# Kernel optimization log

Measured on AMD Instinct MI355X. Metric: run time of the kernel, lower is better.

The kernel has to match this reference:

```python
import jax, jax.numpy as jnp
import numpy as np
import math

B, C, H, W = 8, 64, 256, 256
E, NH = 256, 8
HD = E // NH  # 32


def get_coords(h, w):
    xx, yy = jnp.meshgrid(jnp.arange(h, dtype=jnp.float32), jnp.arange(w, dtype=jnp.float32), indexing='ij')
    return jnp.stack((xx.reshape(-1), yy.reshape(-1)), axis=-1)  # [N, 2]


def setup_inputs() -> dict:
    key = jax.random.key(0)
    ks = jax.random.split(key, 12)
    def xavier(k, shape):
        fan_out, fan_in = shape
        a = math.sqrt(6.0 / (fan_in + fan_out))
        return jax.random.uniform(k, shape, jnp.float32, -a, a)
    x = jax.random.normal(ks[0], (B, C, H, W), jnp.float32)
    z = jax.random.normal(ks[1], (B, C), jnp.float32)
    pos = jax.random.uniform(ks[2], (B, NH, 2), jnp.float32) * (H - 1)
    Wq = xavier(ks[3], (E, C)); bq = jnp.zeros((E,), jnp.float32)
    Wk = xavier(ks[4], (E, C)); bk = jnp.zeros((E,), jnp.float32)
    Wv = xavier(ks[5], (E, C)); bv = jnp.zeros((E,), jnp.float32)
    Wp = xavier(ks[6], (HD, 2)); bp = jax.random.uniform(ks[7], (HD,), jnp.float32, -1.0, 1.0) / math.sqrt(2.0)
    return {"x": x, "z": z, "pos": pos, "Wq": Wq, "bq": bq, "Wk": Wk, "bk": bk,
            "Wv": Wv, "bv": bv, "Wp": Wp, "bp": bp}


def reference(x, z, pos, Wq, bq, Wk, bk, Wv, bv, Wp, bp):
    b, c, h, w = x.shape
    n = h * w
    x_flat = x.reshape(b, c, n).transpose(0, 2, 1)          # [B, N, C]
    pos_grid = get_coords(h, w)                              # [N, 2]
    q = (z @ Wq.T + bq).reshape(b, NH, HD)                   # [B, H, hd]
    k = (x_flat @ Wk.T + bk).reshape(b, n, NH, HD)           # [B, N, H, hd]
    # relative-position modulation of keys
    rel = pos_grid[None, :, None, :] - pos[:, None, :, :]    # [B, N, H, 2]
    qxk = rel @ Wp.T + bp                                    # [B, N, H, hd]
    k = k * qxk
    v = x_flat @ Wv.T + bv                                   # [B, N, E]
    attn_logits = jnp.einsum('bhc,bnhc->bnh', q, k) / math.sqrt(HD)
    attention = jax.nn.softmax(attn_logits, axis=1)          # softmax over N
    pos_out = jnp.einsum('bnh,nx->bhx', attention, pos_grid) # [B, H, 2]
    values = jnp.einsum('bnh,bnc->bhc', attention, v)        # [B, H, E]
    return (values, pos_out)
```

## Files before the change

### kernel.cpp

```cpp
#include <hip/hip_runtime.h>

#define NN    65536
#define NSUB  128
#define NBLK  (NN/NSUB)

typedef short bf16x8 __attribute__((ext_vector_type(8)));
typedef float f32x4v __attribute__((ext_vector_type(4)));
typedef unsigned short ushort_t;
typedef unsigned int uint_t;

#define XSTR   72
#define XHI_B  0
#define XLO_B  18432
#define LGA_B  18432
#define LGSTR  28
#define PSTR   136
#define RED_B  36864
#define SMEM_BYTES 37056

#define WTHI_B  0
#define WTLO_B  32768
#define CJ_B    65536
#define PM_B    66304
#define PL_B    197376
#define PSP_B   328448
#define PSX_B   590592
#define Q_B     8979200
#define QSTR    68

__device__ __forceinline__ uint_t bf16_rne_bits(float f) {
  uint_t u = __float_as_uint(f);
  return (u + 0x7FFFu + ((u >> 16) & 1u)) >> 16;
}
__device__ __forceinline__ uint_t cvt_pk_bf16(float a, float b) {
  uint_t r;
  asm("v_cvt_pk_bf16_f32 %0, %1, %2" : "=v"(r) : "v"(a), "v"(b));
  return r;
}
template <int CTRL>
__device__ __forceinline__ float dpp_add(float x) {
  int t = __builtin_amdgcn_update_dpp(0, __float_as_int(x), CTRL, 0xf, 0xf, false);
  return x + __int_as_float(t);
}
template <int CTRL>
__device__ __forceinline__ float dpp_maxs(float x) {
  int t = __builtin_amdgcn_update_dpp((int)0xFF800000u, __float_as_int(x), CTRL, 0xf, 0xf, false);
  return fmaxf(x, __int_as_float(t));
}
__device__ __forceinline__ float wave_sum(float x) {
  x = dpp_add<0x111>(x); x = dpp_add<0x112>(x); x = dpp_add<0x114>(x);
  x = dpp_add<0x118>(x); x = dpp_add<0x142>(x); x = dpp_add<0x143>(x);
  return __int_as_float(__builtin_amdgcn_readlane(__float_as_int(x), 63));
}
__device__ __forceinline__ float wave_max(float x) {
  x = dpp_maxs<0x111>(x); x = dpp_maxs<0x112>(x); x = dpp_maxs<0x114>(x);
  x = dpp_maxs<0x118>(x); x = dpp_maxs<0x142>(x); x = dpp_maxs<0x143>(x);
  return __int_as_float(__builtin_amdgcn_readlane(__float_as_int(x), 63));
}

__global__ __launch_bounds__(64) void prep_kernel(
    const float* __restrict__ z,  const float* __restrict__ Wq, const float* __restrict__ bq,
    const float* __restrict__ Wk, const float* __restrict__ bk,
    const float* __restrict__ Wp, const float* __restrict__ bp,
    ushort_t* __restrict__ WThi, ushort_t* __restrict__ WTlo, float* __restrict__ Cj)
{
  const int h = blockIdx.x, b = blockIdx.y, t = threadIdx.x;
  __shared__ float q[32];
  if (t < 32) {
    const int e = h*32 + t;
    float a = bq[e];
    const float* zr = z + b*64;
    const float* wr = Wq + e*64;
    #pragma unroll 8
    for (int c = 0; c < 64; ++c) a += zr[c]*wr[c];
    q[t] = a;
  }
  __syncthreads();
  const int c = t;
  float w[3] = {0.f, 0.f, 0.f};
  #pragma unroll 4
  for (int hd = 0; hd < 32; ++hd) {
    const float qk = q[hd] * Wk[(h*32+hd)*64 + c];
    w[0] += qk * bp[hd];
    w[1] += qk * Wp[hd*2+0];
    w[2] += qk * Wp[hd*2+1];
  }
  #pragma unroll
  for (int j = 0; j < 3; ++j) {
    const int coeff = h*3 + j;
    const uint_t hb = bf16_rne_bits(w[j]);
    const float  fh = __uint_as_float(hb << 16);
    const uint_t lb = bf16_rne_bits(w[j] - fh);
    WThi[(b*32 + coeff)*64 + c] = (ushort_t)hb;
    WTlo[(b*32 + coeff)*64 + c] = (ushort_t)lb;
  }
  if (h == 0) {
    #pragma unroll
    for (int r = 0; r < 8; ++r) {
      WThi[(b*32 + 24 + r)*64 + c] = 0;
      WTlo[(b*32 + 24 + r)*64 + c] = 0;
    }
  }
  if (t < 3) {
    float s = 0.f;
    for (int hd = 0; hd < 32; ++hd) {
      const float m = (t == 0) ? bp[hd] : Wp[hd*2 + (t-1)];
      s += q[hd] * m * bk[h*32+hd];
    }
    Cj[b*24 + h*3 + t] = s;
  }
}

__global__ __launch_bounds__(256, 4) void main_kernel(
    const float* __restrict__ x, const float* __restrict__ pos,
    const ushort_t* __restrict__ WThi, const ushort_t* __restrict__ WTlo,
    const float* __restrict__ Cj,
    float* __restrict__ Pm, float* __restrict__ Pl,
    float* __restrict__ Psp, float* __restrict__ Psx)
{
  extern __shared__ char smc[];
  float*    lga = (float*)(smc + LGA_B);
  float*    red = (float*)(smc + RED_B);
  const int t   = threadIdx.x;
  const int blk = blockIdx.x;
  const int b   = blockIdx.y;
  const int n0  = blk * NSUB;
  const int wid = t >> 6, lid = t & 63;
  const int c0  = lid & 15, q4 = lid >> 4;
  const int px  = t & 127;
  const int hgrp = t >> 7;
  const int half = wid & 1;

  bf16x8 bh[2][2], bl[2][2];
  {
    const ushort_t* wtb_h = WThi + b*2048;
    const ushort_t* wtb_l = WTlo + b*2048;
    #pragma unroll
    for (int nt = 0; nt < 2; ++nt)
      #pragma unroll
      for (int ks = 0; ks < 2; ++ks) {
        const int off = (nt*16 + c0)*64 + ks*32 + q4*8;
        bh[nt][ks] = *(const bf16x8*)(wtb_h + off);
        bl[nt][ks] = *(const bf16x8*)(wtb_l + off);
      }
  }

  {
    const int qd  = t & 31;
    const int g   = t >> 5;
    const int swz = (qd >> 1) & 7;
    const int chnk = (g ^ swz) * 16;
    const float* xg = x + (size_t)b*64*NN + (size_t)g*8*NN + n0 + 4*qd;
    f32x4v v[8];
    #pragma unroll
    for (int j = 0; j < 8; ++j) v[j] = *(const f32x4v*)(xg + (size_t)j*NN);
    #pragma unroll
    for (int i = 0; i < 4; ++i) {
      uint_t H[4], L[4];
      #pragma unroll
      for (int jp = 0; jp < 4; ++jp) {
        const float f0 = v[2*jp][i], f1 = v[2*jp+1][i];
        const uint_t hpk = cvt_pk_bf16(f0, f1);
        const float h0 = __uint_as_float(hpk << 16);
        const float h1 = __uint_as_float(hpk & 0xFFFF0000u);
        const uint_t l0 = __float_as_uint(f0 - h0);
        const uint_t l1 = __float_as_uint(f1 - h1);
        H[jp] = hpk;
        L[jp] = __builtin_amdgcn_perm(l1, l0, 0x07060302u);
      }
      char* dh = smc + XHI_B + (4*qd + i)*144 + chnk;
      char* dl = smc + XLO_B + (4*qd + i)*144 + chnk;
      *(uint4*)dh = make_uint4(H[0], H[1], H[2], H[3]);
      *(uint4*)dl = make_uint4(L[0], L[1], L[2], L[3]);
    }
  }

  float cj[12];
  {
    const float* cjp = Cj + b*24 + hgrp*12;
    #pragma unroll
    for (int k = 0; k < 12; ++k) cj[k] = cjp[k];
  }
  const int gx = blk >> 1;
  float rxh[4], py[4];
  #pragma unroll
  for (int hl = 0; hl < 4; ++hl) {
    const int h = hgrp*4 + hl;
    rxh[hl] = (float)gx - pos[(b*8+h)*2 + 0];
    py[hl]  = pos[(b*8+h)*2 + 1];
  }

  __syncthreads();

  f32x4v acc[2][2];
  #pragma unroll
  for (int mt = 0; mt < 2; ++mt) { acc[mt][0] = (f32x4v)0.f; acc[mt][1] = (f32x4v)0.f; }
  {
    const int mrow0 = wid*32;
    #pragma unroll
    for (int mt = 0; mt < 2; ++mt) {
      const int row  = mrow0 + mt*16 + c0;
      const int srow = (4*wid + 2*mt + (c0 >> 3)) & 7;
      const int ch0  = (q4 ^ srow) * 16;
      const char* rh = smc + XHI_B + row*144;
      const char* rl = smc + XLO_B + row*144;
      bf16x8 ah0 = *(const bf16x8*)(rh + ch0);
      bf16x8 ah1 = *(const bf16x8*)(rh + (ch0 ^ 64));
      bf16x8 al0 = *(const bf16x8*)(rl + ch0);
      bf16x8 al1 = *(const bf16x8*)(rl + (ch0 ^ 64));
      #pragma unroll
      for (int nt = 0; nt < 2; ++nt) {
        f32x4v a = acc[mt][nt];
        a = __builtin_amdgcn_mfma_f32_16x16x32_bf16(ah0, bh[nt][0], a, 0, 0, 0);
        a = __builtin_amdgcn_mfma_f32_16x16x32_bf16(ah1, bh[nt][1], a, 0, 0, 0);
        a = __builtin_amdgcn_mfma_f32_16x16x32_bf16(ah0, bl[nt][0], a, 0, 0, 0);
        a = __builtin_amdgcn_mfma_f32_16x16x32_bf16(ah1, bl[nt][1], a, 0, 0, 0);
        a = __builtin_amdgcn_mfma_f32_16x16x32_bf16(al0, bh[nt][0], a, 0, 0, 0);
        a = __builtin_amdgcn_mfma_f32_16x16x32_bf16(al1, bh[nt][1], a, 0, 0, 0);
        acc[mt][nt] = a;
      }
    }
  }
  __syncthreads();

  {
    const int mrow0 = wid*32;
    #pragma unroll
    for (int mt = 0; mt < 2; ++mt)
      #pragma unroll
      for (int r = 0; r < 4; ++r) {
        const int prow = mrow0 + mt*16 + q4*4 + r;
        lga[prow*LGSTR + c0] = acc[mt][0][r];
        if (c0 < 8) lga[prow*LGSTR + 16 + c0] = acc[mt][1][r];
      }
  }
  __syncthreads();

  float a12[12];
  {
    const float4* ap = (const float4*)(lga + px*LGSTR + hgrp*12);
    #pragma unroll
    for (int r = 0; r < 3; ++r) *(float4*)(a12 + 4*r) = ap[r];
  }
  const float tf = (float)(((blk & 1) << 7) + px);
  float lg[4];
  #pragma unroll
  for (int hl = 0; hl < 4; ++hl) {
    const float a0 = a12[hl*3+0] + cj[hl*3+0];
    const float a1 = a12[hl*3+1] + cj[hl*3+1];
    const float a2 = a12[hl*3+2] + cj[hl*3+2];
    lg[hl] = (a0 + rxh[hl]*a1 + (tf - py[hl])*a2) * 0.17677669529663687f;
  }

  #pragma unroll
  for (int hl = 0; hl < 4; ++hl) {
    const float m = wave_max(lg[hl]);
    if (lid == 0) red[(hgrp*4 + hl)*2 + half] = m;
  }
  __syncthreads();

  float p[4];
  #pragma unroll
  for (int hl = 0; hl < 4; ++hl) {
    const int h = hgrp*4 + hl;
    const float M = fmaxf(red[h*2+0], red[h*2+1]);
    p[hl] = __expf(lg[hl] - M);
  }

  {
    ushort_t* pls = (ushort_t*)(smc + LGA_B);
    #pragma unroll
    for (int hl = 0; hl < 4; ++hl) {
      const int h = hgrp*4 + hl;
      const uint_t hb = bf16_rne_bits(p[hl]);
      const float  hf = __uint_as_float(hb << 16);
      const uint_t lb = __float_as_uint(p[hl] - hf) >> 16;
      pls[h*PSTR + px]       = (ushort_t)hb;
      pls[(h+8)*PSTR + px]   = (ushort_t)lb;
    }
  }

  #pragma unroll
  for (int hl = 0; hl < 4; ++hl) {
    const int h = hgrp*4 + hl;
    const float sp  = wave_sum(p[hl]);
    const float spj = wave_sum(p[hl] * tf);
    if (lid == 0) { red[16 + h*2 + half] = sp; red[32 + h*2 + half] = spj; }
  }
  __syncthreads();

  if (t < 8) {
    const int base = (b*NBLK + blk)*8 + t;
    const float M  = fmaxf(red[t*2+0], red[t*2+1]);
    const float L  = red[16+t*2+0] + red[16+t*2+1];
    const float SJ = red[32+t*2+0] + red[32+t*2+1];
    Pm[base] = M;
    Pl[base] = L;
    Psp[base*2+0] = (float)gx * L;
    Psp[base*2+1] = SJ;
  }

  {
    const ushort_t* pls = (const ushort_t*)(smc + LGA_B);
    bf16x8 afr[4];
    #pragma unroll
    for (int ks = 0; ks < 4; ++ks)
      afr[ks] = *(const bf16x8*)(pls + c0*PSTR + ks*32 + q4*8);

    f32x4v accB = (f32x4v)0.f;
    const int chbase = wid*16 + c0;
    const int cbase = (((2*wid + (c0 >> 3)) ^ q4) * 16) + (c0 & 7) * 2;
    #pragma unroll
    for (int ks = 0; ks < 4; ++ks) {
      const char* xc = smc + XHI_B + (ks*32 + q4*8)*144 + (cbase ^ ((ks & 1) * 64));
      bf16x8 bfr;
      #pragma unroll
      for (int i = 0; i < 8; ++i) bfr[i] = *(const short*)(xc + i*144);
      accB = __builtin_amdgcn_mfma_f32_16x16x32_bf16(afr[ks], bfr, accB, 0, 0, 0);
    }

    const size_t pb64 = ((size_t)(b*NBLK + blk))*8*64;
    #pragma unroll
    for (int r = 0; r < 4; ++r) {
      const float o = __shfl_xor(accB[r], 32, 64);
      if (q4 < 2) {
        const int h = q4*4 + r;
        Psx[pb64 + h*64 + chbase] = accB[r] + o;
      }
    }
  }
}

__global__ __launch_bounds__(256) void reduce1_kernel(
    const float* __restrict__ Pm, const float* __restrict__ Pl,
    const float* __restrict__ Psp, const float* __restrict__ Psx,
    float* __restrict__ Q)
{
  const int g = blockIdx.x, h = blockIdx.y, b = blockIdx.z, t = threadIdx.x;
  __shared__ float al[64];
  __shared__ float mgs;
  __shared__ float sums[3];
  __shared__ float sxl[256];
  const int base = (b*NBLK + g*64)*8 + h;

  float m_t = -1e30f;
  if (t < 64) {
    m_t = Pm[base + t*8];
    float mm = m_t;
    #pragma unroll
    for (int off = 32; off >= 1; off >>= 1) mm = fmaxf(mm, __shfl_xor(mm, off, 64));
    if (t == 0) mgs = mm;
  }
  __syncthreads();
  const float Mg = mgs;
  if (t < 64) {
    const float a = __expf(m_t - Mg);
    al[t] = a;
    float lt = Pl[base + t*8] * a;
    float sx = Psp[(base + t*8)*2 + 0] * a;
    float sy = Psp[(base + t*8)*2 + 1] * a;
    #pragma unroll
    for (int off = 32; off >= 1; off >>= 1) {
      lt += __shfl_xor(lt, off, 64);
      sx += __shfl_xor(sx, off, 64);
      sy += __shfl_xor(sy, off, 64);
    }
    if (t == 0) { sums[0] = lt; sums[1] = sx; sums[2] = sy; }
  }
  __syncthreads();
  {
    const int c = t & 63, g2 = t >> 6;
    float acc = 0.f;
    #pragma unroll
    for (int i = 0; i < 16; ++i) {
      const int k = g2*16 + i;
      acc += al[k] * Psx[(size_t)(base + k*8)*64 + c];
    }
    sxl[g2*64 + c] = acc;
  }
  __syncthreads();
  float* q = Q + ((b*8 + h)*8 + g)*QSTR;
  if (t < 64) q[4+t] = sxl[t] + sxl[64+t] + sxl[128+t] + sxl[192+t];
  if (t == 0) { q[0] = Mg; q[1] = sums[0]; q[2] = sums[1]; q[3] = sums[2]; }
}

__global__ __launch_bounds__(64) void reduce2_kernel(
    const float* __restrict__ Q, const float* __restrict__ Wv, const float* __restrict__ bv,
    float* __restrict__ out)
{
  const int h = blockIdx.x, b = blockIdx.y, t = threadIdx.x;
  __shared__ float qm[8], bl[8], l8[8], sx8[8], sy8[8];
  __shared__ float SXs[64];
  const float* qb = Q + ((b*8 + h)*8)*QSTR;

  if (t < 8) qm[t] = qb[t*QSTR + 0];
  __syncthreads();
  float M = qm[0];
  #pragma unroll
  for (int g = 1; g < 8; ++g) M = fmaxf(M, qm[g]);
  if (t < 8) {
    const float be = __expf(qm[t] - M);
    bl[t]  = be;
    l8[t]  = be * qb[t*QSTR + 1];
    sx8[t] = be * qb[t*QSTR + 2];
    sy8[t] = be * qb[t*QSTR + 3];
  }
  __syncthreads();
  float L = 0.f;
  #pragma unroll
  for (int g = 0; g < 8; ++g) L += l8[g];
  const float invL = 1.0f / L;
  {
    float s = 0.f;
    #pragma unroll
    for (int g = 0; g < 8; ++g) s += bl[g] * qb[g*QSTR + 4 + t];
    SXs[t] = s * invL;
  }
  __syncthreads();

  #pragma unroll
  for (int r = 0; r < 4; ++r) {
    const int e = t + 64*r;
    float v = bv[e];
    const float* wvr = Wv + e*64;
    #pragma unroll 8
    for (int c = 0; c < 64; ++c) v += wvr[c] * SXs[c];
    out[(b*8 + h)*256 + e] = v;
  }
  if (t == 0) {
    float spx = 0.f, spy = 0.f;
    #pragma unroll
    for (int g = 0; g < 8; ++g) { spx += sx8[g]; spy += sy8[g]; }
    out[16384 + (b*8 + h)*2 + 0] = spx * invL;
    out[16384 + (b*8 + h)*2 + 1] = spy * invL;
  }
}

extern "C" void kernel_launch(void* const* d_in, const int* in_sizes, int n_in,
                              void* d_out, int out_size, void* d_ws, size_t ws_size,
                              hipStream_t stream)
{
  const float* x   = (const float*)d_in[0];
  const float* z   = (const float*)d_in[1];
  const float* pos = (const float*)d_in[2];
  const float* Wq  = (const float*)d_in[3];
  const float* bq  = (const float*)d_in[4];
  const float* Wk  = (const float*)d_in[5];
  const float* bk  = (const float*)d_in[6];
  const float* Wv  = (const float*)d_in[7];
  const float* bv  = (const float*)d_in[8];
  const float* Wp  = (const float*)d_in[9];
  const float* bp  = (const float*)d_in[10];
  float* out = (float*)d_out;
  char*  wsb = (char*)d_ws;

  ushort_t* WThi = (ushort_t*)(wsb + WTHI_B);
  ushort_t* WTlo = (ushort_t*)(wsb + WTLO_B);
  float* Cj  = (float*)(wsb + CJ_B);
  float* Pm  = (float*)(wsb + PM_B);
  float* Pl  = (float*)(wsb + PL_B);
  float* Psp = (float*)(wsb + PSP_B);
  float* Psx = (float*)(wsb + PSX_B);
  float* Q   = (float*)(wsb + Q_B);

  prep_kernel   <<<dim3(8,8),    64,  0,          stream>>>(z, Wq, bq, Wk, bk, Wp, bp, WThi, WTlo, Cj);
  main_kernel   <<<dim3(NBLK,8), 256, SMEM_BYTES, stream>>>(x, pos, WThi, WTlo, Cj, Pm, Pl, Psp, Psx);
  reduce1_kernel<<<dim3(8,8,8),  256, 0,          stream>>>(Pm, Pl, Psp, Psx, Q);
  reduce2_kernel<<<dim3(8,8),    64,  0,          stream>>>(Q, Wv, bv, out);
}
```

Baseline: 234.8 us.

## Make each wave process its own pixel slice to cut block-wide barriers

Reorganizes main_kernel so each wave loads, converts, projects and computes softmax numerators for its own 32-pixel slice, using a per-wave shared-memory scratch region instead of block-shared staging. This removes three of the five __syncthreads calls. Reductions now use half-wave DPP instead of full-wave reductions with readlane. The P·X MFMA is split per wave across output channel tiles, and the four per-wave partials are summed through shared memory before the final store. The cost is extra shared-memory traffic for that partial sum and more MFMA issues with K=32 each, in exchange for less barrier stalling.

```diff
diff --git a/kernel.cpp b/kernel.cpp
--- a/kernel.cpp
+++ b/kernel.cpp
@@ -9,14 +9,14 @@
 typedef unsigned short ushort_t;
 typedef unsigned int uint_t;
 
-#define XSTR   72
 #define XHI_B  0
 #define XLO_B  18432
-#define LGA_B  18432
+#define SLICE  4608
 #define LGSTR  28
-#define PSTR   136
+#define PSTR   40
+#define PST_OFF 1536
 #define RED_B  36864
-#define SMEM_BYTES 37056
+#define SMEM_BYTES 37248
 
 #define WTHI_B  0
 #define WTLO_B  32768
@@ -37,25 +37,25 @@
   asm("v_cvt_pk_bf16_f32 %0, %1, %2" : "=v"(r) : "v"(a), "v"(b));
   return r;
 }
-template <int CTRL>
+template <int CTRL, int RMASK = 0xf>
 __device__ __forceinline__ float dpp_add(float x) {
-  int t = __builtin_amdgcn_update_dpp(0, __float_as_int(x), CTRL, 0xf, 0xf, false);
+  int t = __builtin_amdgcn_update_dpp(0, __float_as_int(x), CTRL, RMASK, 0xf, false);
   return x + __int_as_float(t);
 }
-template <int CTRL>
+template <int CTRL, int RMASK = 0xf>
 __device__ __forceinline__ float dpp_maxs(float x) {
-  int t = __builtin_amdgcn_update_dpp((int)0xFF800000u, __float_as_int(x), CTRL, 0xf, 0xf, false);
+  int t = __builtin_amdgcn_update_dpp((int)0xFF800000u, __float_as_int(x), CTRL, RMASK, 0xf, false);
   return fmaxf(x, __int_as_float(t));
 }
-__device__ __forceinline__ float wave_sum(float x) {
+__device__ __forceinline__ float half_sum(float x) {
   x = dpp_add<0x111>(x); x = dpp_add<0x112>(x); x = dpp_add<0x114>(x);
-  x = dpp_add<0x118>(x); x = dpp_add<0x142>(x); x = dpp_add<0x143>(x);
-  return __int_as_float(__builtin_amdgcn_readlane(__float_as_int(x), 63));
-}
-__device__ __forceinline__ float wave_max(float x) {
+  x = dpp_add<0x118>(x); x = dpp_add<0x142, 0xA>(x);
+  return x;
+}
+__device__ __forceinline__ float half_max(float x) {
   x = dpp_maxs<0x111>(x); x = dpp_maxs<0x112>(x); x = dpp_maxs<0x114>(x);
-  x = dpp_maxs<0x118>(x); x = dpp_maxs<0x142>(x); x = dpp_maxs<0x143>(x);
-  return __int_as_float(__builtin_amdgcn_readlane(__float_as_int(x), 63));
+  x = dpp_maxs<0x118>(x); x = dpp_maxs<0x142, 0xA>(x);
+  return x;
 }
 
 __global__ __launch_bounds__(64) void prep_kernel(
@@ -119,17 +119,14 @@
     float* __restrict__ Psp, float* __restrict__ Psx)
 {
   extern __shared__ char smc[];
-  float*    lga = (float*)(smc + LGA_B);
-  float*    red = (float*)(smc + RED_B);
+  float* red = (float*)(smc + RED_B);
   const int t   = threadIdx.x;
   const int blk = blockIdx.x;
   const int b   = blockIdx.y;
   const int n0  = blk * NSUB;
-  const int wid = t >> 6, lid = t & 63;
+  const int w   = t >> 6, lid = t & 63;
   const int c0  = lid & 15, q4 = lid >> 4;
-  const int px  = t & 127;
-  const int hgrp = t >> 7;
-  const int half = wid & 1;
+  char* slice = smc + XLO_B + w*SLICE;
 
   bf16x8 bh[2][2], bl[2][2];
   {
@@ -146,11 +143,11 @@
   }
 
   {
-    const int qd  = t & 31;
-    const int g   = t >> 5;
-    const int swz = (qd >> 1) & 7;
+    const int qd  = lid & 7;
+    const int g   = lid >> 3;
+    const int swz = (4*w + (qd >> 1)) & 7;
     const int chnk = (g ^ swz) * 16;
-    const float* xg = x + (size_t)b*64*NN + (size_t)g*8*NN + n0 + 4*qd;
+    const float* xg = x + (size_t)b*64*NN + (size_t)g*8*NN + n0 + w*32 + 4*qd;
     f32x4v v[8];
     #pragma unroll
     for (int j = 0; j < 8; ++j) v[j] = *(const f32x4v*)(xg + (size_t)j*NN);
@@ -168,16 +165,19 @@
         H[jp] = hpk;
         L[jp] = __builtin_amdgcn_perm(l1, l0, 0x07060302u);
       }
-      char* dh = smc + XHI_B + (4*qd + i)*144 + chnk;
-      char* dl = smc + XLO_B + (4*qd + i)*144 + chnk;
+      const int row = w*32 + 4*qd + i;
+      char* dh = smc + XHI_B + row*144 + chnk;
+      char* dl = smc + XLO_B + row*144 + chnk;
       *(uint4*)dh = make_uint4(H[0], H[1], H[2], H[3]);
       *(uint4*)dl = make_uint4(L[0], L[1], L[2], L[3]);
     }
   }
 
+  const int hg  = lid >> 5;
+  const int pxl = lid & 31;
   float cj[12];
   {
-    const float* cjp = Cj + b*24 + hgrp*12;
+    const float* cjp = Cj + b*24 + hg*12;
     #pragma unroll
     for (int k = 0; k < 12; ++k) cj[k] = cjp[k];
   }
@@ -185,22 +185,19 @@
   float rxh[4], py[4];
   #pragma unroll
   for (int hl = 0; hl < 4; ++hl) {
-    const int h = hgrp*4 + hl;
+    const int h = hg*4 + hl;
     rxh[hl] = (float)gx - pos[(b*8+h)*2 + 0];
     py[hl]  = pos[(b*8+h)*2 + 1];
   }
 
-  __syncthreads();
-
   f32x4v acc[2][2];
   #pragma unroll
   for (int mt = 0; mt < 2; ++mt) { acc[mt][0] = (f32x4v)0.f; acc[mt][1] = (f32x4v)0.f; }
   {
-    const int mrow0 = wid*32;
     #pragma unroll
     for (int mt = 0; mt < 2; ++mt) {
-      const int row  = mrow0 + mt*16 + c0;
-      const int srow = (4*wid + 2*mt + (c0 >> 3)) & 7;
+      const int row  = w*32 + mt*16 + c0;
+      const int srow = (4*w + 2*mt + (c0 >> 3)) & 7;
       const int ch0  = (q4 ^ srow) * 16;
       const char* rh = smc + XHI_B + row*144;
       const char* rl = smc + XLO_B + row*144;
@@ -221,28 +218,26 @@
       }
     }
   }
-  __syncthreads();
-
-  {
-    const int mrow0 = wid*32;
+
+  {
+    float* lga_w = (float*)slice;
     #pragma unroll
     for (int mt = 0; mt < 2; ++mt)
       #pragma unroll
       for (int r = 0; r < 4; ++r) {
-        const int prow = mrow0 + mt*16 + q4*4 + r;
-        lga[prow*LGSTR + c0] = acc[mt][0][r];
-        if (c0 < 8) lga[prow*LGSTR + 16 + c0] = acc[mt][1][r];
+        const int prow = mt*16 + q4*4 + r;
+        lga_w[prow*LGSTR + c0] = acc[mt][0][r];
+        if (c0 < 8) lga_w[prow*LGSTR + 16 + c0] = acc[mt][1][r];
       }
   }
-  __syncthreads();
 
   float a12[12];
   {
-    const float4* ap = (const float4*)(lga + px*LGSTR + hgrp*12);
+    const float4* ap = (const float4*)((float*)slice + pxl*LGSTR + hg*12);
     #pragma unroll
     for (int r = 0; r < 3; ++r) *(float4*)(a12 + 4*r) = ap[r];
   }
-  const float tf = (float)(((blk & 1) << 7) + px);
+  const float tf = (float)(((blk & 1) << 7) + w*32 + pxl);
   float lg[4];
   #pragma unroll
   for (int hl = 0; hl < 4; ++hl) {
@@ -254,79 +249,83 @@
 
   #pragma unroll
   for (int hl = 0; hl < 4; ++hl) {
-    const float m = wave_max(lg[hl]);
-    if (lid == 0) red[(hgrp*4 + hl)*2 + half] = m;
+    const float m = half_max(lg[hl]);
+    if ((lid & 31) == 31) red[w*8 + hg*4 + hl] = m;
   }
   __syncthreads();
 
   float p[4];
   #pragma unroll
   for (int hl = 0; hl < 4; ++hl) {
-    const int h = hgrp*4 + hl;
-    const float M = fmaxf(red[h*2+0], red[h*2+1]);
+    const int h = hg*4 + hl;
+    const float M = fmaxf(fmaxf(red[0*8+h], red[1*8+h]), fmaxf(red[2*8+h], red[3*8+h]));
     p[hl] = __expf(lg[hl] - M);
   }
 
-  {
-    ushort_t* pls = (ushort_t*)(smc + LGA_B);
+  #pragma unroll
+  for (int hl = 0; hl < 4; ++hl) {
+    const float sp  = half_sum(p[hl]);
+    const float spj = half_sum(p[hl] * tf);
+    if ((lid & 31) == 31) {
+      red[32 + w*8 + hg*4 + hl] = sp;
+      red[64 + w*8 + hg*4 + hl] = spj;
+    }
+  }
+  {
+    ushort_t* pls = (ushort_t*)slice;
     #pragma unroll
     for (int hl = 0; hl < 4; ++hl) {
-      const int h = hgrp*4 + hl;
+      const int h = hg*4 + hl;
       const uint_t hb = bf16_rne_bits(p[hl]);
       const float  hf = __uint_as_float(hb << 16);
       const uint_t lb = __float_as_uint(p[hl] - hf) >> 16;
-      pls[h*PSTR + px]       = (ushort_t)hb;
-      pls[(h+8)*PSTR + px]   = (ushort_t)lb;
-    }
-  }
-
-  #pragma unroll
-  for (int hl = 0; hl < 4; ++hl) {
-    const int h = hgrp*4 + hl;
-    const float sp  = wave_sum(p[hl]);
-    const float spj = wave_sum(p[hl] * tf);
-    if (lid == 0) { red[16 + h*2 + half] = sp; red[32 + h*2 + half] = spj; }
+      pls[h*PSTR + pxl]     = (ushort_t)hb;
+      pls[(h+8)*PSTR + pxl] = (ushort_t)lb;
+    }
+  }
+
+  {
+    const ushort_t* pls = (const ushort_t*)slice;
+    const bf16x8 afr = *(const bf16x8*)(pls + c0*PSTR + q4*8);
+    const int srow_b = (4*w + q4) & 7;
+    float* pst = (float*)(slice + PST_OFF);
+    #pragma unroll
+    for (int nt = 0; nt < 4; ++nt) {
+      const int gch  = nt*2 + (c0 >> 3);
+      const char* base = smc + XHI_B + (w*32 + q4*8)*144 + ((gch ^ srow_b)*16) + (c0 & 7)*2;
+      bf16x8 bfr;
+      #pragma unroll
+      for (int j = 0; j < 8; ++j) bfr[j] = *(const short*)(base + j*144);
+      f32x4v accB = __builtin_amdgcn_mfma_f32_16x16x32_bf16(afr, bfr, (f32x4v)0.f, 0, 0, 0);
+      #pragma unroll
+      for (int r = 0; r < 4; ++r) {
+        const float o = __shfl_xor(accB[r], 32, 64);
+        if (q4 < 2) pst[(q4*4 + r)*64 + nt*16 + c0] = accB[r] + o;
+      }
+    }
   }
   __syncthreads();
 
   if (t < 8) {
     const int base = (b*NBLK + blk)*8 + t;
-    const float M  = fmaxf(red[t*2+0], red[t*2+1]);
-    const float L  = red[16+t*2+0] + red[16+t*2+1];
-    const float SJ = red[32+t*2+0] + red[32+t*2+1];
+    const float M  = fmaxf(fmaxf(red[0*8+t], red[8+t]), fmaxf(red[16+t], red[24+t]));
+    const float L  = red[32+t] + red[40+t] + red[48+t] + red[56+t];
+    const float SJ = red[64+t] + red[72+t] + red[80+t] + red[88+t];
     Pm[base] = M;
     Pl[base] = L;
     Psp[base*2+0] = (float)gx * L;
     Psp[base*2+1] = SJ;
   }
-
-  {
-    const ushort_t* pls = (const ushort_t*)(smc + LGA_B);
-    bf16x8 afr[4];
-    #pragma unroll
-    for (int ks = 0; ks < 4; ++ks)
-      afr[ks] = *(const bf16x8*)(pls + c0*PSTR + ks*32 + q4*8);
-
-    f32x4v accB = (f32x4v)0.f;
-    const int chbase = wid*16 + c0;
-    const int cbase = (((2*wid + (c0 >> 3)) ^ q4) * 16) + (c0 & 7) * 2;
-    #pragma unroll
-    for (int ks = 0; ks < 4; ++ks) {
-      const char* xc = smc + XHI_B + (ks*32 + q4*8)*144 + (cbase ^ ((ks & 1) * 64));
-      bf16x8 bfr;
-      #pragma unroll
-      for (int i = 0; i < 8; ++i) bfr[i] = *(const short*)(xc + i*144);
-      accB = __builtin_amdgcn_mfma_f32_16x16x32_bf16(afr[ks], bfr, accB, 0, 0, 0);
-    }
-
+  {
     const size_t pb64 = ((size_t)(b*NBLK + blk))*8*64;
     #pragma unroll
-    for (int r = 0; r < 4; ++r) {
-      const float o = __shfl_xor(accB[r], 32, 64);
-      if (q4 < 2) {
-        const int h = q4*4 + r;
-        Psx[pb64 + h*64 + chbase] = accB[r] + o;
-      }
+    for (int r = 0; r < 2; ++r) {
+      const int idx = t + 256*r;
+      float s = 0.f;
+      #pragma unroll
+      for (int w2 = 0; w2 < 4; ++w2)
+        s += *(const float*)(smc + XLO_B + w2*SLICE + PST_OFF + idx*4);
+      Psx[pb64 + idx] = s;
     }
   }
 }
```

Result: no change. 236.8 us (+0.8%).
